# Optimization experiments

Measured on AMD Instinct MI355X. Metric: run time of the kernel, lower is better.

The kernel has to match this reference:

```python
import jax, jax.numpy as jnp
import numpy as np

N_NODES = 100000
N_EDGES = 800000
IN_DIM, HID_DIM, OUT_DIM = 128, 64, 7


def setup_inputs() -> dict:
    key = jax.random.key(0)
    ks = jax.random.split(key, 8)
    x = jax.random.normal(ks[0], (N_NODES, IN_DIM), dtype=jnp.float32)
    edge_index = jax.random.randint(ks[1], (2, N_EDGES), 0, N_NODES, dtype=jnp.int64)
    # Glorot-ish init for weights, zeros for bias (PyG GCNConv default)
    def glorot(k, shape):
        lim = float(np.sqrt(6.0 / (shape[0] + shape[1])))
        return jax.random.uniform(k, shape, dtype=jnp.float32, minval=-lim, maxval=lim)
    return {
        "x": x,
        "edge_index": edge_index,
        "W1": glorot(ks[2], (IN_DIM, HID_DIM)),
        "b1": jnp.zeros((HID_DIM,), jnp.float32),
        "W2": glorot(ks[3], (HID_DIM, HID_DIM)),
        "b2": jnp.zeros((HID_DIM,), jnp.float32),
        "W3": glorot(ks[4], (HID_DIM, OUT_DIM)),
        "b3": jnp.zeros((OUT_DIM,), jnp.float32),
    }


def _gcn_conv(h_in, src, dst, W, b, n_nodes):
    # PyG GCNConv: h = x @ W; add self-loops; D^-1/2 A_hat D^-1/2 aggregation; + b
    h = h_in @ W  # [N, F_out]
    # degree over destination nodes, +1 for self-loop
    deg = jax.ops.segment_sum(jnp.ones_like(dst, dtype=h.dtype), dst,
                              num_segments=n_nodes) + 1.0
    dinv = jax.lax.rsqrt(deg)  # [N]
    coef = dinv[src] * dinv[dst]  # [E]
    msg = h[src] * coef[:, None]  # gather + scale  [E, F_out]
    out = jax.ops.segment_sum(msg, dst, num_segments=n_nodes)  # scatter-add
    out = out + h * (dinv * dinv)[:, None]  # self-loop contribution
    return out + b


def reference(x, edge_index, W1, b1, W2, b2, W3, b3):
    src, dst = edge_index[0], edge_index[1]
    n = x.shape[0]
    h = jax.nn.relu(_gcn_conv(x, src, dst, W1, b1, n))
    # dropout(p=0.5) is identity in eval mode
    h = jax.nn.relu(_gcn_conv(h, src, dst, W2, b2, n))
    return _gcn_conv(h, src, dst, W3, b3, n)
```

## Files before the change

kernel.cpp:

```cpp
#include <hip/hip_runtime.h>

#define N_NODES 100000
#define N_EDGES 800000
#define IN_DIM 128
#define HID 64
#define OUT_DIM 7
#define CAP 48
#define NGROUP 8
#define DSLICE (N_NODES / NGROUP)
#define SUBBLK 390

typedef __bf16 vbf8 __attribute__((ext_vector_type(8)));
typedef float  vf4  __attribute__((ext_vector_type(4)));

__device__ __forceinline__ void wswz_body(int idx, const float* __restrict__ W,
                                          __bf16* __restrict__ out) {
    int j  = idx & 7;
    int l  = (idx >> 3) & 63;
    int nt = (idx >> 9) & 3;
    int ks = idx >> 11;
    int k  = ks * 32 + ((l >> 4) << 3) + j;
    int n  = nt * 16 + (l & 15);
    out[idx] = (__bf16)W[k * 64 + n];
}

__global__ __launch_bounds__(256)
void k_init(const float* __restrict__ W1, __bf16* __restrict__ Wz1,
            const float* __restrict__ W2, __bf16* __restrict__ Wz2) {
    int b = blockIdx.x;
    if (b < 32) wswz_body(b * 256 + threadIdx.x, W1, Wz1);
    else        wswz_body((b - 32) * 256 + threadIdx.x, W2, Wz2);
}

template<int K, bool F32IN>
__device__ __forceinline__ void gemm_mfma_body(int g, int tid,
                                               const void* __restrict__ Xv,
                                               const __bf16* __restrict__ Wswz,
                                               __bf16* __restrict__ Hb) {
    constexpr int KS = K / 32;
    const int lane = tid & 63;
    const int w = g * 4 + (tid >> 6);
    if (w >= N_NODES / 16) return;
    const int r0 = w * 16;
    const int m = lane & 15;
    const int quad = lane >> 4;

    vbf8 bfrag[KS][4];
    const vbf8* wp = (const vbf8*)Wswz;
    #pragma unroll
    for (int ks = 0; ks < KS; ++ks)
        #pragma unroll
        for (int nt = 0; nt < 4; ++nt)
            bfrag[ks][nt] = wp[(ks * 4 + nt) * 64 + lane];

    vf4 acc[4] = {};
    #pragma unroll
    for (int ks = 0; ks < KS; ++ks) {
        vbf8 a;
        if (F32IN) {
            const float* xp = (const float*)Xv + (size_t)(r0 + m) * K + ks * 32 + quad * 8;
            float4 f0 = *(const float4*)xp;
            float4 f1 = *(const float4*)(xp + 4);
            a[0] = (__bf16)f0.x; a[1] = (__bf16)f0.y; a[2] = (__bf16)f0.z; a[3] = (__bf16)f0.w;
            a[4] = (__bf16)f1.x; a[5] = (__bf16)f1.y; a[6] = (__bf16)f1.z; a[7] = (__bf16)f1.w;
        } else {
            a = *(const vbf8*)((const __bf16*)Xv + (size_t)(r0 + m) * K + ks * 32 + quad * 8);
        }
        #pragma unroll
        for (int nt = 0; nt < 4; ++nt)
            acc[nt] = __builtin_amdgcn_mfma_f32_16x16x32_bf16(a, bfrag[ks][nt], acc[nt], 0, 0, 0);
    }

    #pragma unroll
    for (int nt = 0; nt < 4; ++nt)
        #pragma unroll
        for (int r = 0; r < 4; ++r)
            Hb[(size_t)(r0 + quad * 4 + r) * 64 + nt * 16 + m] = (__bf16)acc[nt][r];
}

#define FILL_BLKS (NGROUP * SUBBLK)
#define GEMM_BLKS ((N_NODES / 16 + 3) / 4)
__global__ __launch_bounds__(256)
void k_build_gemm1(const int* __restrict__ ei, int* __restrict__ cnt,
                   int* __restrict__ csr, const float* __restrict__ X,
                   const __bf16* __restrict__ Wz1, __bf16* __restrict__ Hb) {
    int b = blockIdx.x;
    if (b < FILL_BLKS) {
        int group = b & 7, sub = b >> 3;
        int lo = group * DSLICE;
        for (int e = sub * 256 + threadIdx.x; e < N_EDGES; e += SUBBLK * 256) {
            int d = ei[N_EDGES + e];
            if ((unsigned)(d - lo) < (unsigned)DSLICE) {
                int s = ei[e];
                int pos = atomicAdd(&cnt[d], 1);
                if (pos < CAP) csr[(size_t)d * CAP + pos] = s;
            }
        }
    } else {
        gemm_mfma_body<IN_DIM, true>(b - FILL_BLKS, threadIdx.x, X, Wz1, Hb);
    }
}

__global__ __launch_bounds__(256)
void k_gemm2(const __bf16* __restrict__ Ab, const __bf16* __restrict__ Wz2,
             __bf16* __restrict__ Hb) {
    gemm_mfma_body<HID, false>(blockIdx.x, threadIdx.x, Ab, Wz2, Hb);
}

__global__ __launch_bounds__(256)
void k_gather64(const int* __restrict__ cnt, const int* __restrict__ csr,
                const float* __restrict__ bias, const __bf16* __restrict__ Hb,
                __bf16* __restrict__ Ab) {
    int node = blockIdx.x * 32 + (threadIdx.x >> 3);
    int q = threadIdx.x & 7;
    if (node >= N_NODES) return;
    int deg = cnt[node];
    int end = deg < CAP ? deg : CAP;
    float dd = rsqrtf((float)deg + 1.0f);
    float d2 = dd * dd;
    vbf8 h8 = *(const vbf8*)(Hb + (size_t)node * 64 + q * 8);
    float4 b0 = *(const float4*)(bias + q * 8);
    float4 b1 = *(const float4*)(bias + q * 8 + 4);
    float acc[8];
    acc[0] = fmaf((float)h8[0], d2, b0.x); acc[1] = fmaf((float)h8[1], d2, b0.y);
    acc[2] = fmaf((float)h8[2], d2, b0.z); acc[3] = fmaf((float)h8[3], d2, b0.w);
    acc[4] = fmaf((float)h8[4], d2, b1.x); acc[5] = fmaf((float)h8[5], d2, b1.y);
    acc[6] = fmaf((float)h8[6], d2, b1.z); acc[7] = fmaf((float)h8[7], d2, b1.w);
    const int* row = csr + (size_t)node * CAP;
    int j = 0;
    for (; j + 2 <= end; j += 2) {
        int s0 = row[j];
        int s1 = row[j + 1];
        float c0 = rsqrtf((float)cnt[s0] + 1.0f) * dd;
        float c1 = rsqrtf((float)cnt[s1] + 1.0f) * dd;
        vbf8 v0 = *(const vbf8*)(Hb + (size_t)s0 * 64 + q * 8);
        vbf8 v1 = *(const vbf8*)(Hb + (size_t)s1 * 64 + q * 8);
        #pragma unroll
        for (int t = 0; t < 8; ++t) acc[t] = fmaf((float)v0[t], c0, acc[t]);
        #pragma unroll
        for (int t = 0; t < 8; ++t) acc[t] = fmaf((float)v1[t], c1, acc[t]);
    }
    if (j < end) {
        int s = row[j];
        float c = rsqrtf((float)cnt[s] + 1.0f) * dd;
        vbf8 v = *(const vbf8*)(Hb + (size_t)s * 64 + q * 8);
        #pragma unroll
        for (int t = 0; t < 8; ++t) acc[t] = fmaf((float)v[t], c, acc[t]);
    }
    vbf8 o;
    #pragma unroll
    for (int t = 0; t < 8; ++t) o[t] = (__bf16)fmaxf(acc[t], 0.f);
    *(vbf8*)(Ab + (size_t)node * 64 + q * 8) = o;
}

__global__ __launch_bounds__(256)
void k_gemm3(const __bf16* __restrict__ Ab, const float* __restrict__ W,
             const float* __restrict__ bias, const int* __restrict__ cnt,
             float* __restrict__ S, float* __restrict__ Out) {
    int row = blockIdx.x * blockDim.x + threadIdx.x;
    if (row >= N_NODES) return;
    float c[7] = {};
    const vbf8* xr = (const vbf8*)(Ab + (size_t)row * 64);
    #pragma unroll
    for (int k0 = 0; k0 < 8; ++k0) {
        vbf8 a = xr[k0];
        #pragma unroll
        for (int t = 0; t < 8; ++t) {
            float av = (float)a[t];
            #pragma unroll
            for (int j = 0; j < 7; ++j)
                c[j] = fmaf(av, W[(size_t)(k0 * 8 + t) * 7 + j], c[j]);
        }
    }
    float dd = rsqrtf((float)cnt[row] + 1.0f);
    float d2 = dd * dd;
    #pragma unroll
    for (int j = 0; j < 7; ++j) {
        S[(size_t)row * 7 + j] = c[j];
        Out[(size_t)row * 7 + j] = fmaf(c[j], d2, bias[j]);
    }
}

__global__ __launch_bounds__(256)
void k_gather7(const int* __restrict__ cnt, const int* __restrict__ csr,
               const float* __restrict__ S, float* __restrict__ Out) {
    int node = blockIdx.x * 32 + (threadIdx.x >> 3);
    int j7 = threadIdx.x & 7;
    if (node >= N_NODES || j7 >= 7) return;
    int deg = cnt[node];
    int end = deg < CAP ? deg : CAP;
    float dd = rsqrtf((float)deg + 1.0f);
    const int* rowp = csr + (size_t)node * CAP;
    float acc = Out[(size_t)node * 7 + j7];
    for (int j = 0; j < end; ++j) {
        int s = rowp[j];
        float c = rsqrtf((float)cnt[s] + 1.0f) * dd;
        acc = fmaf(S[(size_t)s * 7 + j7], c, acc);
    }
    Out[(size_t)node * 7 + j7] = acc;
}

static inline size_t align256(size_t x) { return (x + 255) & ~(size_t)255; }

extern "C" void kernel_launch(void* const* d_in, const int* in_sizes, int n_in,
                              void* d_out, int out_size, void* d_ws, size_t ws_size,
                              hipStream_t stream) {
    const float* x  = (const float*)d_in[0];
    const int*   ei = (const int*)d_in[1];
    const float* W1 = (const float*)d_in[2];
    const float* b1 = (const float*)d_in[3];
    const float* W2 = (const float*)d_in[4];
    const float* b2 = (const float*)d_in[5];
    const float* W3 = (const float*)d_in[6];
    const float* b3 = (const float*)d_in[7];
    float* out = (float*)d_out;

    char* wsp = (char*)d_ws;
    int*    cnt   = (int*)wsp;    wsp += align256(sizeof(int) * N_NODES);
    int*    csr   = (int*)wsp;    wsp += align256(sizeof(int) * (size_t)N_NODES * CAP);
    __bf16* Wz1   = (__bf16*)wsp; wsp += align256(sizeof(__bf16) * IN_DIM * 64);
    __bf16* Wz2   = (__bf16*)wsp; wsp += align256(sizeof(__bf16) * HID * 64);
    __bf16* bufHb = (__bf16*)wsp; wsp += align256(sizeof(__bf16) * (size_t)N_NODES * 64);
    __bf16* Ab    = (__bf16*)wsp; wsp += align256(sizeof(__bf16) * (size_t)N_NODES * 64);
    float*  bufS  = (float*)wsp;  wsp += align256(sizeof(float) * (size_t)N_NODES * 7);

    const int nb_g = N_NODES / 32;
    const int nb_n = (N_NODES + 255) / 256;

    hipMemsetAsync(cnt, 0, sizeof(int) * N_NODES, stream);
    k_init<<<48, 256, 0, stream>>>(W1, Wz1, W2, Wz2);

    k_build_gemm1<<<FILL_BLKS + GEMM_BLKS, 256, 0, stream>>>(ei, cnt, csr, x, Wz1, bufHb);
    k_gather64<<<nb_g, 256, 0, stream>>>(cnt, csr, b1, bufHb, Ab);

    k_gemm2<<<GEMM_BLKS, 256, 0, stream>>>(Ab, Wz2, bufHb);
    k_gather64<<<nb_g, 256, 0, stream>>>(cnt, csr, b2, bufHb, Ab);

    k_gemm3<<<nb_n, 256, 0, stream>>>(Ab, W3, b3, cnt, bufS, out);
    k_gather7<<<nb_g, 256, 0, stream>>>(cnt, csr, bufS, out);
}
```

Baseline: 231.1 us.

## Fuse neighbor gathers with following GEMMs via shared memory and fold memset into init

Merges each 64-wide aggregation with the next layer's GEMM (MFMA for layer 2, scalar 7-wide for layer 3), staging the aggregated rows in LDS so they are never written to and reread from global memory. The memset of the degree counts moves into the init kernel, and the CSR build reads destination indices as int4. Together this removes two kernel launches and two full round trips of the intermediate activations. The cost is heavier blocks with LDS use: the layer-3 block holds 256 rows, about 36KB, which may lower occupancy for the latency-bound gathers.

```diff
diff --git a/kernel.cpp b/kernel.cpp
--- a/kernel.cpp
+++ b/kernel.cpp
@@ -9,6 +9,7 @@
 #define NGROUP 8
 #define DSLICE (N_NODES / NGROUP)
 #define SUBBLK 390
+#define NB_N ((N_NODES + 255) / 256)
 
 typedef __bf16 vbf8 __attribute__((ext_vector_type(8)));
 typedef float  vf4  __attribute__((ext_vector_type(4)));
@@ -25,19 +26,24 @@
 }
 
 __global__ __launch_bounds__(256)
-void k_init(const float* __restrict__ W1, __bf16* __restrict__ Wz1,
-            const float* __restrict__ W2, __bf16* __restrict__ Wz2) {
+void k_init(int* __restrict__ cnt, const float* __restrict__ W1,
+            __bf16* __restrict__ Wz1, const float* __restrict__ W2,
+            __bf16* __restrict__ Wz2) {
     int b = blockIdx.x;
-    if (b < 32) wswz_body(b * 256 + threadIdx.x, W1, Wz1);
-    else        wswz_body((b - 32) * 256 + threadIdx.x, W2, Wz2);
-}
-
-template<int K, bool F32IN>
-__device__ __forceinline__ void gemm_mfma_body(int g, int tid,
-                                               const void* __restrict__ Xv,
-                                               const __bf16* __restrict__ Wswz,
-                                               __bf16* __restrict__ Hb) {
-    constexpr int KS = K / 32;
+    if (b < NB_N) {
+        int i = b * 256 + threadIdx.x;
+        if (i < N_NODES) cnt[i] = 0;
+    } else if (b < NB_N + 32) {
+        wswz_body((b - NB_N) * 256 + threadIdx.x, W1, Wz1);
+    } else {
+        wswz_body((b - NB_N - 32) * 256 + threadIdx.x, W2, Wz2);
+    }
+}
+
+__device__ __forceinline__ void gemm1_body(int g, int tid, const float* __restrict__ X,
+                                           const __bf16* __restrict__ Wswz,
+                                           __bf16* __restrict__ Hb) {
+    constexpr int K = IN_DIM, KS = K / 32;
     const int lane = tid & 63;
     const int w = g * 4 + (tid >> 6);
     if (w >= N_NODES / 16) return;
@@ -56,21 +62,16 @@
     vf4 acc[4] = {};
     #pragma unroll
     for (int ks = 0; ks < KS; ++ks) {
+        const float* xp = X + (size_t)(r0 + m) * K + ks * 32 + quad * 8;
+        float4 f0 = *(const float4*)xp;
+        float4 f1 = *(const float4*)(xp + 4);
         vbf8 a;
-        if (F32IN) {
-            const float* xp = (const float*)Xv + (size_t)(r0 + m) * K + ks * 32 + quad * 8;
-            float4 f0 = *(const float4*)xp;
-            float4 f1 = *(const float4*)(xp + 4);
-            a[0] = (__bf16)f0.x; a[1] = (__bf16)f0.y; a[2] = (__bf16)f0.z; a[3] = (__bf16)f0.w;
-            a[4] = (__bf16)f1.x; a[5] = (__bf16)f1.y; a[6] = (__bf16)f1.z; a[7] = (__bf16)f1.w;
-        } else {
-            a = *(const vbf8*)((const __bf16*)Xv + (size_t)(r0 + m) * K + ks * 32 + quad * 8);
-        }
+        a[0] = (__bf16)f0.x; a[1] = (__bf16)f0.y; a[2] = (__bf16)f0.z; a[3] = (__bf16)f0.w;
+        a[4] = (__bf16)f1.x; a[5] = (__bf16)f1.y; a[6] = (__bf16)f1.z; a[7] = (__bf16)f1.w;
         #pragma unroll
         for (int nt = 0; nt < 4; ++nt)
             acc[nt] = __builtin_amdgcn_mfma_f32_16x16x32_bf16(a, bfrag[ks][nt], acc[nt], 0, 0, 0);
     }
-
     #pragma unroll
     for (int nt = 0; nt < 4; ++nt)
         #pragma unroll
@@ -88,32 +89,29 @@
     if (b < FILL_BLKS) {
         int group = b & 7, sub = b >> 3;
         int lo = group * DSLICE;
-        for (int e = sub * 256 + threadIdx.x; e < N_EDGES; e += SUBBLK * 256) {
-            int d = ei[N_EDGES + e];
-            if ((unsigned)(d - lo) < (unsigned)DSLICE) {
-                int s = ei[e];
-                int pos = atomicAdd(&cnt[d], 1);
-                if (pos < CAP) csr[(size_t)d * CAP + pos] = s;
-            }
+        const int4* dst4 = (const int4*)(ei + N_EDGES);
+        for (int e4 = sub * 256 + threadIdx.x; e4 < N_EDGES / 4; e4 += SUBBLK * 256) {
+            int4 d4 = dst4[e4];
+            bool m0 = (unsigned)(d4.x - lo) < (unsigned)DSLICE;
+            bool m1 = (unsigned)(d4.y - lo) < (unsigned)DSLICE;
+            bool m2 = (unsigned)(d4.z - lo) < (unsigned)DSLICE;
+            bool m3 = (unsigned)(d4.w - lo) < (unsigned)DSLICE;
+            if (!(m0 | m1 | m2 | m3)) continue;
+            int e = e4 * 4;
+            if (m0) { int s = ei[e];     int p = atomicAdd(&cnt[d4.x], 1); if (p < CAP) csr[(size_t)d4.x * CAP + p] = s; }
+            if (m1) { int s = ei[e + 1]; int p = atomicAdd(&cnt[d4.y], 1); if (p < CAP) csr[(size_t)d4.y * CAP + p] = s; }
+            if (m2) { int s = ei[e + 2]; int p = atomicAdd(&cnt[d4.z], 1); if (p < CAP) csr[(size_t)d4.z * CAP + p] = s; }
+            if (m3) { int s = ei[e + 3]; int p = atomicAdd(&cnt[d4.w], 1); if (p < CAP) csr[(size_t)d4.w * CAP + p] = s; }
         }
     } else {
-        gemm_mfma_body<IN_DIM, true>(b - FILL_BLKS, threadIdx.x, X, Wz1, Hb);
-    }
-}
-
-__global__ __launch_bounds__(256)
-void k_gemm2(const __bf16* __restrict__ Ab, const __bf16* __restrict__ Wz2,
-             __bf16* __restrict__ Hb) {
-    gemm_mfma_body<HID, false>(blockIdx.x, threadIdx.x, Ab, Wz2, Hb);
-}
-
-__global__ __launch_bounds__(256)
-void k_gather64(const int* __restrict__ cnt, const int* __restrict__ csr,
-                const float* __restrict__ bias, const __bf16* __restrict__ Hb,
-                __bf16* __restrict__ Ab) {
-    int node = blockIdx.x * 32 + (threadIdx.x >> 3);
-    int q = threadIdx.x & 7;
-    if (node >= N_NODES) return;
+        gemm1_body(b - FILL_BLKS, threadIdx.x, X, Wz1, Hb);
+    }
+}
+
+__device__ __forceinline__ vbf8 gather_body(int node, int q, const int* __restrict__ cnt,
+                                            const int* __restrict__ csr,
+                                            const float* __restrict__ bias,
+                                            const __bf16* __restrict__ Hb) {
     int deg = cnt[node];
     int end = deg < CAP ? deg : CAP;
     float dd = rsqrtf((float)deg + 1.0f);
@@ -129,8 +127,7 @@
     const int* row = csr + (size_t)node * CAP;
     int j = 0;
     for (; j + 2 <= end; j += 2) {
-        int s0 = row[j];
-        int s1 = row[j + 1];
+        int s0 = row[j], s1 = row[j + 1];
         float c0 = rsqrtf((float)cnt[s0] + 1.0f) * dd;
         float c1 = rsqrtf((float)cnt[s1] + 1.0f) * dd;
         vbf8 v0 = *(const vbf8*)(Hb + (size_t)s0 * 64 + q * 8);
@@ -150,34 +147,97 @@
     vbf8 o;
     #pragma unroll
     for (int t = 0; t < 8; ++t) o[t] = (__bf16)fmaxf(acc[t], 0.f);
-    *(vbf8*)(Ab + (size_t)node * 64 + q * 8) = o;
-}
-
-__global__ __launch_bounds__(256)
-void k_gemm3(const __bf16* __restrict__ Ab, const float* __restrict__ W,
-             const float* __restrict__ bias, const int* __restrict__ cnt,
-             float* __restrict__ S, float* __restrict__ Out) {
-    int row = blockIdx.x * blockDim.x + threadIdx.x;
-    if (row >= N_NODES) return;
+    return o;
+}
+
+__global__ __launch_bounds__(256)
+void k_gather_gemm2(const int* __restrict__ cnt, const int* __restrict__ csr,
+                    const float* __restrict__ b1, const __bf16* __restrict__ HbA,
+                    const __bf16* __restrict__ Wz2, __bf16* __restrict__ HbB) {
+    __shared__ __bf16 abuf[64][72];
+    const int tid = threadIdx.x;
+    const int lane = tid & 63;
+    const int node0 = blockIdx.x * 64;
+
+    vbf8 bfrag[2][4];
+    const vbf8* wp = (const vbf8*)Wz2;
+    #pragma unroll
+    for (int ks = 0; ks < 2; ++ks)
+        #pragma unroll
+        for (int nt = 0; nt < 4; ++nt)
+            bfrag[ks][nt] = wp[(ks * 4 + nt) * 64 + lane];
+
+    #pragma unroll
+    for (int p = 0; p < 2; ++p) {
+        int nl = p * 32 + (tid >> 3);
+        int node = node0 + nl;
+        int q = tid & 7;
+        if (node < N_NODES)
+            *(vbf8*)&abuf[nl][q * 8] = gather_body(node, q, cnt, csr, b1, HbA);
+    }
+    __syncthreads();
+
+    const int w = tid >> 6;
+    const int m = lane & 15;
+    const int quad = lane >> 4;
+    const int rl = w * 16 + m;
+    vf4 acc[4] = {};
+    #pragma unroll
+    for (int ks = 0; ks < 2; ++ks) {
+        vbf8 a = *(const vbf8*)&abuf[rl][ks * 32 + quad * 8];
+        #pragma unroll
+        for (int nt = 0; nt < 4; ++nt)
+            acc[nt] = __builtin_amdgcn_mfma_f32_16x16x32_bf16(a, bfrag[ks][nt], acc[nt], 0, 0, 0);
+    }
+    #pragma unroll
+    for (int nt = 0; nt < 4; ++nt)
+        #pragma unroll
+        for (int r = 0; r < 4; ++r) {
+            int row = node0 + w * 16 + quad * 4 + r;
+            if (row < N_NODES)
+                HbB[(size_t)row * 64 + nt * 16 + m] = (__bf16)acc[nt][r];
+        }
+}
+
+__global__ __launch_bounds__(256)
+void k_gather_gemm3(const int* __restrict__ cnt, const int* __restrict__ csr,
+                    const float* __restrict__ b2, const __bf16* __restrict__ HbB,
+                    const float* __restrict__ W3, const float* __restrict__ b3,
+                    float* __restrict__ S, float* __restrict__ Out) {
+    __shared__ __bf16 abuf[256][72];
+    const int tid = threadIdx.x;
+    const int node0 = blockIdx.x * 256;
+
+    #pragma unroll
+    for (int p = 0; p < 8; ++p) {
+        int nl = p * 32 + (tid >> 3);
+        int node = node0 + nl;
+        int q = tid & 7;
+        if (node < N_NODES)
+            *(vbf8*)&abuf[nl][q * 8] = gather_body(node, q, cnt, csr, b2, HbB);
+    }
+    __syncthreads();
+
+    int node = node0 + tid;
+    if (node >= N_NODES) return;
     float c[7] = {};
-    const vbf8* xr = (const vbf8*)(Ab + (size_t)row * 64);
     #pragma unroll
     for (int k0 = 0; k0 < 8; ++k0) {
-        vbf8 a = xr[k0];
+        vbf8 a = *(const vbf8*)&abuf[tid][k0 * 8];
         #pragma unroll
         for (int t = 0; t < 8; ++t) {
             float av = (float)a[t];
             #pragma unroll
             for (int j = 0; j < 7; ++j)
-                c[j] = fmaf(av, W[(size_t)(k0 * 8 + t) * 7 + j], c[j]);
+                c[j] = fmaf(av, W3[(size_t)(k0 * 8 + t) * 7 + j], c[j]);
         }
     }
-    float dd = rsqrtf((float)cnt[row] + 1.0f);
+    float dd = rsqrtf((float)cnt[node] + 1.0f);
     float d2 = dd * dd;
     #pragma unroll
     for (int j = 0; j < 7; ++j) {
-        S[(size_t)row * 7 + j] = c[j];
-        Out[(size_t)row * 7 + j] = fmaf(c[j], d2, bias[j]);
+        S[(size_t)node * 7 + j] = c[j];
+        Out[(size_t)node * 7 + j] = fmaf(c[j], d2, b3[j]);
     }
 }
 
@@ -216,26 +276,17 @@
     float* out = (float*)d_out;
 
     char* wsp = (char*)d_ws;
-    int*    cnt   = (int*)wsp;    wsp += align256(sizeof(int) * N_NODES);
-    int*    csr   = (int*)wsp;    wsp += align256(sizeof(int) * (size_t)N_NODES * CAP);
-    __bf16* Wz1   = (__bf16*)wsp; wsp += align256(sizeof(__bf16) * IN_DIM * 64);
-    __bf16* Wz2   = (__bf16*)wsp; wsp += align256(sizeof(__bf16) * HID * 64);
-    __bf16* bufHb = (__bf16*)wsp; wsp += align256(sizeof(__bf16) * (size_t)N_NODES * 64);
-    __bf16* Ab    = (__bf16*)wsp; wsp += align256(sizeof(__bf16) * (size_t)N_NODES * 64);
-    float*  bufS  = (float*)wsp;  wsp += align256(sizeof(float) * (size_t)N_NODES * 7);
-
-    const int nb_g = N_NODES / 32;
-    const int nb_n = (N_NODES + 255) / 256;
-
-    hipMemsetAsync(cnt, 0, sizeof(int) * N_NODES, stream);
-    k_init<<<48, 256, 0, stream>>>(W1, Wz1, W2, Wz2);
-
-    k_build_gemm1<<<FILL_BLKS + GEMM_BLKS, 256, 0, stream>>>(ei, cnt, csr, x, Wz1, bufHb);
-    k_gather64<<<nb_g, 256, 0, stream>>>(cnt, csr, b1, bufHb, Ab);
-
-    k_gemm2<<<GEMM_BLKS, 256, 0, stream>>>(Ab, Wz2, bufHb);
-    k_gather64<<<nb_g, 256, 0, stream>>>(cnt, csr, b2, bufHb, Ab);
-
-    k_gemm3<<<nb_n, 256, 0, stream>>>(Ab, W3, b3, cnt, bufS, out);
-    k_gather7<<<nb_g, 256, 0, stream>>>(cnt, csr, bufS, out);
-}
+    int*    cnt  = (int*)wsp;    wsp += align256(sizeof(int) * N_NODES);
+    int*    csr  = (int*)wsp;    wsp += align256(sizeof(int) * (size_t)N_NODES * CAP);
+    __bf16* Wz1  = (__bf16*)wsp; wsp += align256(sizeof(__bf16) * IN_DIM * 64);
+    __bf16* Wz2  = (__bf16*)wsp; wsp += align256(sizeof(__bf16) * HID * 64);
+    __bf16* HbA  = (__bf16*)wsp; wsp += align256(sizeof(__bf16) * (size_t)N_NODES * 64);
+    __bf16* HbB  = (__bf16*)wsp; wsp += align256(sizeof(__bf16) * (size_t)N_NODES * 64);
+    float*  bufS = (float*)wsp;  wsp += align256(sizeof(float) * (size_t)N_NODES * 7);
+
+    k_init<<<NB_N + 48, 256, 0, stream>>>(cnt, W1, Wz1, W2, Wz2);
+    k_build_gemm1<<<FILL_BLKS + GEMM_BLKS, 256, 0, stream>>>(ei, cnt, csr, x, Wz1, HbA);
+    k_gather_gemm2<<<(N_NODES + 63) / 64, 256, 0, stream>>>(cnt, csr, b1, HbA, Wz2, HbB);
+    k_gather_gemm3<<<NB_N, 256, 0, stream>>>(cnt, csr, b2, HbB, W3, b3, bufS, out);
+    k_gather7<<<N_NODES / 32, 256, 0, stream>>>(cnt, csr, bufS, out);
+}
```

After: 247.3 us. 7.0% more time.
